# Kernel optimization log

Measured on AMD Instinct MI355X. Metric: run time of the kernel, lower is better.

The kernel has to match this reference:

```python
import jax, jax.numpy as jnp
import numpy as np


def conv1x1(x, w, b):
    # x: (B,C,H,W), w: (O,C), b: (O,) -- 1x1 conv == channel matmul
    return jnp.einsum('bchw,oc->bohw', x, w) + b[None, :, None, None]


def setup_inputs() -> dict:
    key = jax.random.key(0)
    B, C, H, W = 4, 256, 64, 64
    Ch = C // 2
    ks = jax.random.split(key, 12)
    s = 0.05
    return {
        'x':    jax.random.normal(ks[0], (B, C, H, W), jnp.float32),
        'wf1':  jax.random.normal(ks[1], (Ch, C), jnp.float32) * s,
        'bf1':  jnp.zeros((Ch,), jnp.float32),
        'wf2':  jax.random.normal(ks[2], (Ch, Ch), jnp.float32) * s,
        'bf2':  jnp.zeros((Ch,), jnp.float32),
        'wg1':  jax.random.normal(ks[3], (Ch, C), jnp.float32) * s,
        'bg1':  jnp.zeros((Ch,), jnp.float32),
        'wg2':  jax.random.normal(ks[4], (Ch, Ch), jnp.float32) * s,
        'bg2':  jnp.zeros((Ch,), jnp.float32),
        'wh':   jax.random.normal(ks[5], (C, C), jnp.float32) * s,
        'bh':   jnp.zeros((C,), jnp.float32),
        'gamma': jnp.full((1,), 0.5, jnp.float32),
    }


def reference(x, wf1, bf1, wf2, bf2, wg1, bg1, wg2, bg2, wh, bh, gamma):
    B, C, H, W = x.shape
    N = H * W
    # f_ and g_: conv1x1 -> relu -> conv1x1, projecting C -> C/2
    f = conv1x1(jax.nn.relu(conv1x1(x, wf1, bf1)), wf2, bf2).reshape(B, -1, N)  # (B,C/2,N)
    g = conv1x1(jax.nn.relu(conv1x1(x, wg1, bg1)), wg2, bg2).reshape(B, -1, N)  # (B,C/2,N)
    h = conv1x1(x, wh, bh).reshape(B, C, N)                                     # (B,C,N)
    # attn_dist = bmm(f^T, g): (B, N, N)
    attn = jnp.einsum('bcn,bcm->bnm', f, g)
    # softmax over dim=1 (the query axis) -- non-standard axis, as in source
    attn_soft = jax.nn.softmax(attn, axis=1)
    out = jnp.einsum('bcn,bnm->bcm', h, attn_soft).reshape(B, C, H, W)
    out = gamma[0] * out + x  # skip connection
    return out, attn_soft.reshape(B, H, W, N)
```

## Files before the change

### kernel.cpp

```cpp
#include <hip/hip_runtime.h>

typedef unsigned short u16;
typedef unsigned int   u32;
typedef float  floatx4 __attribute__((ext_vector_type(4)));
typedef __bf16 bfx8    __attribute__((ext_vector_type(8)));
typedef u16    u16x8   __attribute__((ext_vector_type(8)));

#define DEV __device__ __forceinline__

#define NB 4
#define NC 256
#define NCH 128
#define NSP 4096
#define OUT_OFF 4194304

DEV u16 f2bf(float f) {
  u32 u = __builtin_bit_cast(u32, f);
  u = (u + 0x7fffu + ((u >> 16) & 1u)) >> 16;
  return (u16)u;
}

DEV void lds_load16(const u16* g, u16* l) {
  __builtin_amdgcn_global_load_lds(
      (const __attribute__((address_space(1))) u32*)g,
      (__attribute__((address_space(3))) u32*)l, 16, 0, 0);
}

DEV floatx4 mfma16(bfx8 a, bfx8 b, floatx4 c) {
  return __builtin_amdgcn_mfma_f32_16x16x32_bf16(a, b, c, 0, 0, 0);
}

DEV float rsum16(float v) {
  #pragma unroll
  for (int m = 1; m < 16; m <<= 1) v += __shfl_xor(v, m, 64);
  return v;
}

__global__ __launch_bounds__(256) void cvt_all(
    const float* __restrict__ wf1, const float* __restrict__ wg1,
    const float* __restrict__ wf2, const float* __restrict__ wg2,
    const float* __restrict__ wh,
    u16* __restrict__ wfg1b, u16* __restrict__ wfg2b, u16* __restrict__ whb) {
  int i = blockIdx.x * 256 + threadIdx.x;
  if (i < 32768) { wfg1b[i] = f2bf(wf1[i]); return; }
  i -= 32768;
  if (i < 32768) { wfg1b[32768 + i] = f2bf(wg1[i]); return; }
  i -= 32768;
  if (i < 16384) { wfg2b[i] = f2bf(wf2[i]); return; }
  i -= 16384;
  if (i < 16384) { wfg2b[16384 + i] = f2bf(wg2[i]); return; }
  i -= 16384;
  whb[i] = f2bf(wh[i]);
}

__global__ __launch_bounds__(256) void prep_k(
    float* __restrict__ rs,
    const float* __restrict__ bf1, const float* __restrict__ bg1,
    const float* __restrict__ bf2, const float* __restrict__ bg2,
    float* __restrict__ bfg1, float* __restrict__ bfg2) {
  int i = blockIdx.x * 256 + threadIdx.x;
  if (i < NB * NSP) { rs[i] = 0.f; return; }
  i -= NB * NSP;
  if (i < 128) { bfg1[i] = bf1[i]; return; }
  i -= 128;
  if (i < 128) { bfg1[128 + i] = bg1[i]; return; }
  i -= 128;
  if (i < 128) { bfg2[i] = bf2[i]; return; }
  i -= 128;
  if (i < 128) { bfg2[128 + i] = bg2[i]; return; }
}

__global__ __launch_bounds__(256) void transpose_x(const float* __restrict__ x,
                                                   u16* __restrict__ xT) {
  __shared__ float T[64 * 65];
  const int b = blockIdx.z, c0 = blockIdx.y * 64, n0 = blockIdx.x * 64;
  const int tid = threadIdx.x;
  const int j = tid & 63, r0 = tid >> 6;
  const size_t xbase = ((size_t)b * NC + c0) * NSP + n0;
  #pragma unroll
  for (int s = 0; s < 16; s++) {
    int cl = s * 4 + r0;
    T[cl * 65 + j] = x[xbase + (size_t)cl * NSP + j];
  }
  __syncthreads();
  const size_t tbase = ((size_t)b * NSP + n0) * NC + c0;
  #pragma unroll
  for (int s = 0; s < 16; s++) {
    int nr = s * 4 + r0;
    xT[tbase + (size_t)nr * NC + j] = f2bf(T[j * 65 + nr]);
  }
}

template<int BM, int BN, int BK, int BIAS, bool RELU, bool OUTBF16, bool FINAL,
         bool SWZ>
__global__ __launch_bounds__(256) void gemm_bt_k(
    const u16* __restrict__ A, long long sA, int lda,
    const u16* __restrict__ Bt, long long sB, int ldb,
    void* __restrict__ C, long long sC, int ldc,
    int K, const float* __restrict__ bias, int sbias,
    const float* __restrict__ gamma, const float* __restrict__ xres,
    const float* __restrict__ rsv) {
  constexpr int TM = BM / 32, TN = BN / 32, KS = BK / 32;
  __shared__ u16 As[BM * BK];
  __shared__ u16 Bs[BN * BK];
  int bx = blockIdx.x, by = blockIdx.y, bz = blockIdx.z;
  if constexpr (SWZ) {
    const int gx = gridDim.x, gy = gridDim.y;
    const int nwg = gx * gy * gridDim.z;
    const int bid = (bz * gy + by) * gx + bx;
    const int lx = (bid & 7) * (nwg >> 3) + (bid >> 3);
    bx = lx % gx;
    const int t = lx / gx;
    by = t % gy;
    bz = t / gy;
  }
  const int b = bz;
  const u16* Ab = A + (size_t)sA * b;
  const u16* Bb = Bt + (size_t)sB * b;
  const int m0 = bx * BM, n0 = by * BN;
  const int tid = threadIdx.x, lane = tid & 63, wave = tid >> 6;
  const int q = lane >> 4, cc = lane & 15;
  const int wm = (wave >> 1) * (BM / 2), wn = (wave & 1) * (BN / 2);

  floatx4 acc[TM][TN];
  #pragma unroll
  for (int mi = 0; mi < TM; mi++)
    #pragma unroll
    for (int ni = 0; ni < TN; ni++)
      acc[mi][ni] = floatx4{0.f, 0.f, 0.f, 0.f};

  for (int k0 = 0; k0 < K; k0 += BK) {
    #pragma unroll
    for (int i = 0; i < BM * BK / 2048; i++) {
      int slot = i * 256 + tid;
      int fr = slot / (64 * KS);
      int ks = (slot / 64) % KS;
      int qq = (slot >> 4) & 3, cq = slot & 15;
      lds_load16(Ab + (size_t)(m0 + fr * 16 + cq) * lda + k0 + ks * 32 + qq * 8,
                 As + slot * 8);
    }
    #pragma unroll
    for (int i = 0; i < BN * BK / 2048; i++) {
      int slot = i * 256 + tid;
      int fr = slot / (64 * KS);
      int ks = (slot / 64) % KS;
      int qq = (slot >> 4) & 3, cq = slot & 15;
      lds_load16(Bb + (size_t)(n0 + fr * 16 + cq) * ldb + k0 + ks * 32 + qq * 8,
                 Bs + slot * 8);
    }
    __syncthreads();
    #pragma unroll
    for (int ks = 0; ks < KS; ks++) {
      bfx8 af[TM], bfr[TN];
      #pragma unroll
      for (int mi = 0; mi < TM; mi++)
        af[mi] = *(const bfx8*)(As + ((((wm >> 4) + mi) * KS + ks) * 64 + lane) * 8);
      #pragma unroll
      for (int ni = 0; ni < TN; ni++)
        bfr[ni] = *(const bfx8*)(Bs + ((((wn >> 4) + ni) * KS + ks) * 64 + lane) * 8);
      #pragma unroll
      for (int mi = 0; mi < TM; mi++)
        #pragma unroll
        for (int ni = 0; ni < TN; ni++)
          acc[mi][ni] = mfma16(af[mi], bfr[ni], acc[mi][ni]);
    }
    __syncthreads();
  }

  float g0 = 0.f;
  if constexpr (FINAL) g0 = gamma[0];
  #pragma unroll
  for (int mi = 0; mi < TM; mi++) {
    #pragma unroll
    for (int ni = 0; ni < TN; ni++) {
      const int col = n0 + wn + ni * 16 + cc;
      float scl = 0.f;
      if constexpr (FINAL) scl = g0 / rsv[(size_t)b * NSP + col];
      #pragma unroll
      for (int r = 0; r < 4; r++) {
        int row = m0 + wm + mi * 16 + q * 4 + r;
        float v = acc[mi][ni][r];
        if constexpr (BIAS == 1) v += bias[b * sbias + col];
        if constexpr (BIAS == 2) v += bias[b * sbias + row];
        if constexpr (RELU) v = fmaxf(v, 0.f);
        size_t idx = (size_t)sC * b + (size_t)row * ldc + col;
        if constexpr (FINAL) v = v * scl + xres[idx];
        if constexpr (OUTBF16) ((u16*)C)[idx] = f2bf(v);
        else ((float*)C)[idx] = v;
      }
    }
  }
}

__global__ __launch_bounds__(256) void attn_se_k(
    const u16* __restrict__ gT, const u16* __restrict__ fT,
    float* __restrict__ rsum, u16* __restrict__ pT) {
  __shared__ u16 Bs[64 * 128];
  __shared__ u16 Pb[64 * 72];
  const int b = blockIdx.z, m0 = blockIdx.y * 64, n0 = blockIdx.x * 512;
  const int tid = threadIdx.x, lane = tid & 63, wave = tid >> 6;
  const int q = lane >> 4, cc = lane & 15;
  const size_t bN = (size_t)b * NSP;

  bfx8 af[4];
  {
    const u16* gA = gT + (bN + m0 + wave * 16 + cc) * NCH;
    #pragma unroll
    for (int ks = 0; ks < 4; ks++) af[ks] = *(const bfx8*)(gA + ks * 32 + q * 8);
  }
  float ps[4] = {0.f, 0.f, 0.f, 0.f};

  for (int sc = 0; sc < 8; sc++) {
    const int nc = n0 + sc * 64;
    #pragma unroll
    for (int i = 0; i < 4; i++) {
      int slot = i * 256 + tid;
      int ni = slot >> 8, ks = (slot >> 6) & 3;
      int qq = (slot >> 4) & 3, cq = slot & 15;
      lds_load16(fT + (bN + nc + ni * 16 + cq) * NCH + ks * 32 + qq * 8,
                 Bs + slot * 8);
    }
    __syncthreads();
    #pragma unroll
    for (int ni = 0; ni < 4; ni++) {
      floatx4 s = floatx4{0.f, 0.f, 0.f, 0.f};
      #pragma unroll
      for (int ks = 0; ks < 4; ks++) {
        bfx8 bfr = *(const bfx8*)(Bs + ((ni * 4 + ks) * 64 + lane) * 8);
        s = mfma16(af[ks], bfr, s);
      }
      #pragma unroll
      for (int r = 0; r < 4; r++) {
        float e = __expf(fminf(s[r], 80.f));
        ps[r] += e;
        Pb[(wave * 16 + q * 4 + r) * 72 + ni * 16 + cc] = f2bf(e);
      }
    }
    __syncthreads();
    #pragma unroll
    for (int i = 0; i < 2; i++) {
      int slot = i * 256 + tid;
      int ml = slot >> 3, c8 = slot & 7;
      u16x8 v = *(const u16x8*)(Pb + ml * 72 + c8 * 8);
      *(u16x8*)(pT + (bN + m0 + ml) * NSP + nc + c8 * 8) = v;
    }
  }
  #pragma unroll
  for (int r = 0; r < 4; r++) ps[r] = rsum16(ps[r]);
  if (cc == 0) {
    #pragma unroll
    for (int r = 0; r < 4; r++)
      atomicAdd(&rsum[bN + m0 + wave * 16 + q * 4 + r], ps[r]);
  }
}

__global__ __launch_bounds__(256) void attn_norm_k(
    const u16* __restrict__ pT, const float* __restrict__ rs,
    float* __restrict__ outP) {
  __shared__ float T[64 * 65];
  const int b = blockIdx.z, n0 = blockIdx.x * 64, m0 = blockIdx.y * 64;
  const int tid = threadIdx.x;
  const size_t bN = (size_t)b * NSP;
  #pragma unroll
  for (int i = 0; i < 2; i++) {
    int slot = i * 256 + tid;
    int ml = slot >> 3, c8 = slot & 7;
    u16x8 v = *(const u16x8*)(pT + (bN + m0 + ml) * NSP + n0 + c8 * 8);
    float rinv = 1.f / rs[bN + m0 + ml];
    #pragma unroll
    for (int j = 0; j < 8; j++) {
      u32 w = (u32)v[j] << 16;
      T[ml * 65 + c8 * 8 + j] = __builtin_bit_cast(float, w) * rinv;
    }
  }
  __syncthreads();
  #pragma unroll
  for (int i = 0; i < 4; i++) {
    int slot = i * 256 + tid;
    int nl = slot >> 4, f4 = slot & 15;
    floatx4 o;
    #pragma unroll
    for (int k = 0; k < 4; k++) o[k] = T[(f4 * 4 + k) * 65 + nl];
    *(floatx4*)(outP + (bN + n0 + nl) * NSP + m0 + f4 * 4) = o;
  }
}

extern "C" void kernel_launch(void* const* d_in, const int* in_sizes, int n_in,
                              void* d_out, int out_size, void* d_ws, size_t ws_size,
                              hipStream_t stream) {
  const float* x     = (const float*)d_in[0];
  const float* wf1   = (const float*)d_in[1];
  const float* bf1   = (const float*)d_in[2];
  const float* wf2   = (const float*)d_in[3];
  const float* bf2   = (const float*)d_in[4];
  const float* wg1   = (const float*)d_in[5];
  const float* bg1   = (const float*)d_in[6];
  const float* wg2   = (const float*)d_in[7];
  const float* bg2   = (const float*)d_in[8];
  const float* wh    = (const float*)d_in[9];
  const float* bh    = (const float*)d_in[10];
  const float* gamma = (const float*)d_in[11];
  float* out = (float*)d_out;

  char* ws = (char*)d_ws;
  size_t off = 0;
  auto alloc = [&](size_t bytes) -> char* {
    char* p = ws + off;
    off += (bytes + 255) & ~(size_t)255;
    return p;
  };
  u16* wfg1b = (u16*)alloc((size_t)256 * 256 * 2);
  u16* wfg2b = (u16*)alloc((size_t)2 * 128 * 128 * 2);
  u16* whb   = (u16*)alloc((size_t)NC * NC * 2);
  float* bfg1 = (float*)alloc(256 * 4);
  float* bfg2 = (float*)alloc(256 * 4);
  u16* xT   = (u16*)alloc((size_t)NB * NSP * NC * 2);
  u16* fg1T = (u16*)alloc((size_t)NB * NSP * 256 * 2);
  u16* fTb  = (u16*)alloc((size_t)NB * NSP * NCH * 2);
  u16* gTb  = (u16*)alloc((size_t)NB * NSP * NCH * 2);
  u16* hb   = (u16*)alloc((size_t)NB * NC * NSP * 2);
  float* rs = (float*)alloc((size_t)NB * NSP * 4);
  u16* pTb  = (u16*)alloc((size_t)NB * NSP * NSP * 2);

  cvt_all<<<dim3(640), 256, 0, stream>>>(wf1, wg1, wf2, wg2, wh,
                                         wfg1b, wfg2b, whb);
  prep_k<<<dim3(66), 256, 0, stream>>>(rs, bf1, bg1, bf2, bg2, bfg1, bfg2);
  transpose_x<<<dim3(NSP / 64, NC / 64, NB), 256, 0, stream>>>(x, xT);

  const long long sX = (long long)NSP * NC;
  const long long sH = (long long)NC * NSP;
  const long long sP = (long long)NSP * NSP;
  const long long sFG = (long long)NB * NSP * NCH;

  gemm_bt_k<64, 128, 64, 1, true, true, false, false>
      <<<dim3(256, 2, 1), 256, 0, stream>>>(
      xT, 0, NC, wfg1b, 0, NC, fg1T, 0, 256, NC, bfg1, 0,
      nullptr, nullptr, nullptr);
  gemm_bt_k<64, 128, 64, 1, false, true, false, false>
      <<<dim3(256, 1, 2), 256, 0, stream>>>(
      fg1T, 128, 256, wfg2b, 128 * 128, NCH, fTb, sFG, NCH, NCH, bfg2, 128,
      nullptr, nullptr, nullptr);
  gemm_bt_k<64, 128, 64, 2, false, true, false, false>
      <<<dim3(4, 32, NB), 256, 0, stream>>>(
      whb, 0, NC, xT, sX, NC, hb, sH, NSP, NC, bh, 0,
      nullptr, nullptr, nullptr);

  attn_se_k<<<dim3(8, 64, NB), 256, 0, stream>>>(gTb, fTb, rs, pTb);

  gemm_bt_k<128, 64, 64, 0, false, false, true, true>
      <<<dim3(2, 64, NB), 256, 0, stream>>>(
      hb, sH, NSP, pTb, sP, NSP, out, sH, NSP, NSP, nullptr, 0,
      gamma, x, rs);

  attn_norm_k<<<dim3(NSP / 64, NSP / 64, NB), 256, 0, stream>>>(
      pTb, rs, out + OUT_OFF);

  (void)in_sizes; (void)n_in; (void)out_size; (void)ws_size;
}
```

Measured before the change: 495.9 us.

## Double-buffer GEMM LDS tiles, merge prep kernels, widen attention-normalize tiles

The GEMM kernel now ping-pongs between two LDS buffers, so the global→LDS loads for the next K tile are issued before the MFMAs on the current one. This overlaps load latency with compute and drops one barrier per iteration, at the cost of twice the LDS per block. The weight-conversion and bias/rowsum-init kernels are merged into one launch to save launch overhead. The attention normalize/transpose kernel now handles 64x256 tiles: it keeps bf16 in LDS and applies precomputed reciprocals on the way out, which halves LDS traffic and lengthens each contiguous output row.

```diff
diff --git a/kernel.cpp b/kernel.cpp
--- a/kernel.cpp
+++ b/kernel.cpp
@@ -20,6 +20,11 @@
   return (u16)u;
 }
 
+DEV float bf2f(u16 h) {
+  u32 w = (u32)h << 16;
+  return __builtin_bit_cast(float, w);
+}
+
 DEV void lds_load16(const u16* g, u16* l) {
   __builtin_amdgcn_global_load_lds(
       (const __attribute__((address_space(1))) u32*)g,
@@ -40,7 +45,11 @@
     const float* __restrict__ wf1, const float* __restrict__ wg1,
     const float* __restrict__ wf2, const float* __restrict__ wg2,
     const float* __restrict__ wh,
-    u16* __restrict__ wfg1b, u16* __restrict__ wfg2b, u16* __restrict__ whb) {
+    u16* __restrict__ wfg1b, u16* __restrict__ wfg2b, u16* __restrict__ whb,
+    float* __restrict__ rs,
+    const float* __restrict__ bf1, const float* __restrict__ bg1,
+    const float* __restrict__ bf2, const float* __restrict__ bg2,
+    float* __restrict__ bfg1, float* __restrict__ bfg2) {
   int i = blockIdx.x * 256 + threadIdx.x;
   if (i < 32768) { wfg1b[i] = f2bf(wf1[i]); return; }
   i -= 32768;
@@ -50,15 +59,8 @@
   i -= 16384;
   if (i < 16384) { wfg2b[16384 + i] = f2bf(wg2[i]); return; }
   i -= 16384;
-  whb[i] = f2bf(wh[i]);
-}
-
-__global__ __launch_bounds__(256) void prep_k(
-    float* __restrict__ rs,
-    const float* __restrict__ bf1, const float* __restrict__ bg1,
-    const float* __restrict__ bf2, const float* __restrict__ bg2,
-    float* __restrict__ bfg1, float* __restrict__ bfg2) {
-  int i = blockIdx.x * 256 + threadIdx.x;
+  if (i < 65536) { whb[i] = f2bf(wh[i]); return; }
+  i -= 65536;
   if (i < NB * NSP) { rs[i] = 0.f; return; }
   i -= NB * NSP;
   if (i < 128) { bfg1[i] = bf1[i]; return; }
@@ -101,8 +103,9 @@
     const float* __restrict__ gamma, const float* __restrict__ xres,
     const float* __restrict__ rsv) {
   constexpr int TM = BM / 32, TN = BN / 32, KS = BK / 32;
-  __shared__ u16 As[BM * BK];
-  __shared__ u16 Bs[BN * BK];
+  constexpr int ASZ = BM * BK, BSZ = BN * BK;
+  __shared__ u16 As[2][ASZ];
+  __shared__ u16 Bs[2][BSZ];
   int bx = blockIdx.x, by = blockIdx.y, bz = blockIdx.z;
   if constexpr (SWZ) {
     const int gx = gridDim.x, gy = gridDim.y;
@@ -122,42 +125,48 @@
   const int q = lane >> 4, cc = lane & 15;
   const int wm = (wave >> 1) * (BM / 2), wn = (wave & 1) * (BN / 2);
 
-  floatx4 acc[TM][TN];
-  #pragma unroll
-  for (int mi = 0; mi < TM; mi++)
-    #pragma unroll
-    for (int ni = 0; ni < TN; ni++)
-      acc[mi][ni] = floatx4{0.f, 0.f, 0.f, 0.f};
-
-  for (int k0 = 0; k0 < K; k0 += BK) {
-    #pragma unroll
-    for (int i = 0; i < BM * BK / 2048; i++) {
+  auto stage = [&](int p, int k0) {
+    #pragma unroll
+    for (int i = 0; i < ASZ / 2048; i++) {
       int slot = i * 256 + tid;
       int fr = slot / (64 * KS);
       int ks = (slot / 64) % KS;
       int qq = (slot >> 4) & 3, cq = slot & 15;
       lds_load16(Ab + (size_t)(m0 + fr * 16 + cq) * lda + k0 + ks * 32 + qq * 8,
-                 As + slot * 8);
-    }
-    #pragma unroll
-    for (int i = 0; i < BN * BK / 2048; i++) {
+                 &As[p][slot * 8]);
+    }
+    #pragma unroll
+    for (int i = 0; i < BSZ / 2048; i++) {
       int slot = i * 256 + tid;
       int fr = slot / (64 * KS);
       int ks = (slot / 64) % KS;
       int qq = (slot >> 4) & 3, cq = slot & 15;
       lds_load16(Bb + (size_t)(n0 + fr * 16 + cq) * ldb + k0 + ks * 32 + qq * 8,
-                 Bs + slot * 8);
-    }
-    __syncthreads();
+                 &Bs[p][slot * 8]);
+    }
+  };
+
+  floatx4 acc[TM][TN];
+  #pragma unroll
+  for (int mi = 0; mi < TM; mi++)
+    #pragma unroll
+    for (int ni = 0; ni < TN; ni++)
+      acc[mi][ni] = floatx4{0.f, 0.f, 0.f, 0.f};
+
+  stage(0, 0);
+  __syncthreads();
+  int p = 0;
+  for (int k0 = 0; k0 < K; k0 += BK) {
+    if (k0 + BK < K) stage(p ^ 1, k0 + BK);
     #pragma unroll
     for (int ks = 0; ks < KS; ks++) {
       bfx8 af[TM], bfr[TN];
       #pragma unroll
       for (int mi = 0; mi < TM; mi++)
-        af[mi] = *(const bfx8*)(As + ((((wm >> 4) + mi) * KS + ks) * 64 + lane) * 8);
+        af[mi] = *(const bfx8*)(&As[p][((((wm >> 4) + mi) * KS + ks) * 64 + lane) * 8]);
       #pragma unroll
       for (int ni = 0; ni < TN; ni++)
-        bfr[ni] = *(const bfx8*)(Bs + ((((wn >> 4) + ni) * KS + ks) * 64 + lane) * 8);
+        bfr[ni] = *(const bfx8*)(&Bs[p][((((wn >> 4) + ni) * KS + ks) * 64 + lane) * 8]);
       #pragma unroll
       for (int mi = 0; mi < TM; mi++)
         #pragma unroll
@@ -165,6 +174,7 @@
           acc[mi][ni] = mfma16(af[mi], bfr[ni], acc[mi][ni]);
     }
     __syncthreads();
+    p ^= 1;
   }
 
   float g0 = 0.f;
@@ -257,30 +267,31 @@
 __global__ __launch_bounds__(256) void attn_norm_k(
     const u16* __restrict__ pT, const float* __restrict__ rs,
     float* __restrict__ outP) {
-  __shared__ float T[64 * 65];
-  const int b = blockIdx.z, n0 = blockIdx.x * 64, m0 = blockIdx.y * 64;
+  __shared__ u16 T[64 * 257];
+  __shared__ float rinvs[256];
+  const int b = blockIdx.z, n0 = blockIdx.x * 64, m0 = blockIdx.y * 256;
   const int tid = threadIdx.x;
   const size_t bN = (size_t)b * NSP;
-  #pragma unroll
-  for (int i = 0; i < 2; i++) {
+
+  rinvs[tid] = 1.f / rs[bN + m0 + tid];
+  #pragma unroll
+  for (int i = 0; i < 8; i++) {
     int slot = i * 256 + tid;
-    int ml = slot >> 3, c8 = slot & 7;
-    u16x8 v = *(const u16x8*)(pT + (bN + m0 + ml) * NSP + n0 + c8 * 8);
-    float rinv = 1.f / rs[bN + m0 + ml];
-    #pragma unroll
-    for (int j = 0; j < 8; j++) {
-      u32 w = (u32)v[j] << 16;
-      T[ml * 65 + c8 * 8 + j] = __builtin_bit_cast(float, w) * rinv;
-    }
+    int mi = slot >> 3, c8 = slot & 7;
+    u16x8 v = *(const u16x8*)(pT + (bN + m0 + mi) * NSP + n0 + c8 * 8);
+    #pragma unroll
+    for (int j = 0; j < 8; j++) T[(c8 * 8 + j) * 257 + mi] = v[j];
   }
   __syncthreads();
   #pragma unroll
-  for (int i = 0; i < 4; i++) {
+  for (int i = 0; i < 16; i++) {
     int slot = i * 256 + tid;
-    int nl = slot >> 4, f4 = slot & 15;
+    int nl = slot >> 6, f4 = slot & 63;
+    floatx4 rv = *(const floatx4*)(rinvs + f4 * 4);
+    const u16* tr = T + nl * 257 + f4 * 4;
     floatx4 o;
     #pragma unroll
-    for (int k = 0; k < 4; k++) o[k] = T[(f4 * 4 + k) * 65 + nl];
+    for (int k = 0; k < 4; k++) o[k] = bf2f(tr[k]) * rv[k];
     *(floatx4*)(outP + (bN + n0 + nl) * NSP + m0 + f4 * 4) = o;
   }
 }
@@ -322,9 +333,9 @@
   float* rs = (float*)alloc((size_t)NB * NSP * 4);
   u16* pTb  = (u16*)alloc((size_t)NB * NSP * NSP * 2);
 
-  cvt_all<<<dim3(640), 256, 0, stream>>>(wf1, wg1, wf2, wg2, wh,
-                                         wfg1b, wfg2b, whb);
-  prep_k<<<dim3(66), 256, 0, stream>>>(rs, bf1, bg1, bf2, bg2, bfg1, bfg2);
+  cvt_all<<<dim3(707), 256, 0, stream>>>(wf1, wg1, wf2, wg2, wh,
+                                         wfg1b, wfg2b, whb,
+                                         rs, bf1, bg1, bf2, bg2, bfg1, bfg2);
   transpose_x<<<dim3(NSP / 64, NC / 64, NB), 256, 0, stream>>>(x, xT);
 
   const long long sX = (long long)NSP * NC;
@@ -352,7 +363,7 @@
       hb, sH, NSP, pTb, sP, NSP, out, sH, NSP, NSP, nullptr, 0,
       gamma, x, rs);
 
-  attn_norm_k<<<dim3(NSP / 64, NSP / 64, NB), 256, 0, stream>>>(
+  attn_norm_k<<<dim3(NSP / 64, NSP / 256, NB), 256, 0, stream>>>(
       pTb, rs, out + OUT_OFF);
 
   (void)in_sizes; (void)n_in; (void)out_size; (void)ws_size;
```

Result: no change. 494.9 us (-0.2%).
